# Performance work log

Measured on AMD Instinct MI355X. Metric: run time of the kernel, lower is better.

The kernel has to match this reference:

```python
import jax, jax.numpy as jnp
import numpy as np

G = 2            # num_codevector_groups
C = 320          # num_codevectors_per_group
VQ_DIM = 256     # codevector_dim
HID = 512        # conv_dimensions[-1]
TAU = 2.0


def setup_inputs() -> dict:
    key = jax.random.key(0)
    k1, k2, k3, k4 = jax.random.split(key, 4)
    B, S = 16, 2048
    x = jax.random.normal(k1, (B, S, HID), dtype=jnp.float32)
    # iid Gumbel(0,1) noise, same shape as flattened logits [B*S*G, C]
    u = jax.random.uniform(k2, (B * S * G, C), dtype=jnp.float32, minval=1e-6, maxval=1.0 - 1e-6)
    gumbel = -jnp.log(-jnp.log(u))
    Wq = jax.random.normal(k3, (G * C, HID), dtype=jnp.float32) * (1.0 / np.sqrt(HID))
    bq = jnp.zeros((G * C,), dtype=jnp.float32)
    codevectors = jax.random.uniform(k4, (1, G * C, VQ_DIM // G), dtype=jnp.float32)
    return {"x": x, "gumbel": gumbel, "Wq": Wq, "bq": bq, "codevectors": codevectors}


def reference(x, gumbel, Wq, bq, codevectors):
    B, S, H = x.shape
    N = B * S
    logits = jnp.einsum('bsh,gh->bsg', x, Wq) + bq          # [B, S, G*C]
    logits = logits.reshape(N * G, C)

    # hard gumbel-softmax (training path) with straight-through estimator
    y_soft = jax.nn.softmax((logits + gumbel) / TAU, axis=-1)
    idx = jnp.argmax(y_soft, axis=-1)
    y_hard = jax.nn.one_hot(idx, C, dtype=y_soft.dtype)
    probs = y_hard + y_soft - jax.lax.stop_gradient(y_soft)  # [N*G, C]

    # perplexity from plain softmax of logits (no gumbel noise), masked_token_idx=None
    soft_probs = jax.nn.softmax(logits.reshape(N, G, C), axis=-1)
    mean_p = soft_probs.mean(axis=0)                          # [G, C]
    perplexity = jnp.exp(-jnp.sum(mean_p * jnp.log(mean_p + 1e-7), axis=-1)).sum()

    # weighted sum over codes per group == einsum (same math as broadcast*sum in torch)
    cv = codevectors.reshape(G, C, VQ_DIM // G)               # [G, C, d]
    sel = jnp.einsum('ngc,gcd->ngd', probs.reshape(N, G, C), cv)
    selected_codes = sel.reshape(B, S, VQ_DIM)
    return selected_codes, perplexity
```

## Files before the change

kernel.cpp:

```cpp
#include <hip/hip_runtime.h>
#include <hip/hip_fp16.h>

#define HID 512
#define GC  640
#define CC  320
#define GG  2
#define DHALF 128
#define MARGIN 0.004f
#define FB 4

typedef __attribute__((ext_vector_type(8))) _Float16 half8;
typedef __attribute__((ext_vector_type(4))) float float4v;

__device__ __forceinline__ void gload16(const void* g, void* l) {
    __builtin_amdgcn_global_load_lds(
        (const __attribute__((address_space(1))) void*)(unsigned long long)g,
        (__attribute__((address_space(3))) void*)(unsigned)(unsigned long long)l,
        16, 0, 0);
}

__global__ __launch_bounds__(256) void zero_misc(float* meanAcc, int* cnt) {
    for (int i = threadIdx.x; i < GC; i += 256) meanAcc[i] = 0.f;
    if (threadIdx.x < 2) cnt[threadIdx.x] = 0;
}

__global__ __launch_bounds__(256) void convert_f16(
    const float* __restrict__ in, unsigned short* __restrict__ out, int n8)
{
    int i = blockIdx.x * 256 + threadIdx.x;
    if (i >= n8) return;
    const float4* p = (const float4*)in + (size_t)i * 2;
    float4 v0 = p[0], v1 = p[1];
    float f[8] = {v0.x, v0.y, v0.z, v0.w, v1.x, v1.y, v1.z, v1.w};
    unsigned r[4];
#pragma unroll
    for (int j = 0; j < 4; ++j) {
        __half2 hh = __float22half2_rn(make_float2(f[2*j], f[2*j+1]));
        r[j] = __builtin_bit_cast(unsigned, hh);
    }
    uint4 o = {r[0], r[1], r[2], r[3]};
    *(uint4*)(out + (size_t)i * 8) = o;
}

__global__ __launch_bounds__(512, 4) void fused(
    const float* __restrict__ X, const unsigned short* __restrict__ Wh,
    const float* __restrict__ bq, const float* __restrict__ gum,
    const float* __restrict__ cv, float* __restrict__ out,
    float* __restrict__ meanAcc, int* __restrict__ cnt,
    int* __restrict__ flags0, int* __restrict__ flags1)
{
    __shared__ __align__(16) unsigned short As[2][4096];
    __shared__ __align__(16) unsigned short Bs[2][10240];
    __shared__ float bqs[CC];
    __shared__ float smean[CC];

    const int tid  = threadIdx.x;
    const int lane = tid & 63;
    const int wid  = tid >> 6;
    const int lq   = lane & 15;
    const int q    = lane >> 4;

    int bid = blockIdx.x;
    int nwg = gridDim.x;
    int swz = ((nwg & 7) == 0) ? (bid & 7) * (nwg >> 3) + (bid >> 3) : bid;
    const int g    = swz & 1;
    const int tok0 = (swz >> 1) * 128;
    int* flagsg = g ? flags1 : flags0;

    for (int i = tid; i < CC; i += 512) { bqs[i] = bq[g * CC + i]; smean[i] = 0.f; }

    const int iss0 = wid, iss1 = wid + 8, iss2 = wid + 16;
    const int c0 = (iss0 * 64 + lane) ^ (((iss0 * 64 + lane) >> 3) & 7);
    const int c1 = (iss1 * 64 + lane) ^ (((iss1 * 64 + lane) >> 3) & 7);
    const int c2 = (iss2 * 64 + lane) ^ (((iss2 * 64 + lane) >> 3) & 7);
    const unsigned short* srcB0 = Wh + ((size_t)(g * CC + (c0 >> 2))) * HID + (c0 & 3) * 8;
    const unsigned short* srcB1 = Wh + ((size_t)(g * CC + (c1 >> 2))) * HID + (c1 & 3) * 8;
    const unsigned short* srcB2 = Wh + ((size_t)(g * CC + (c2 >> 2))) * HID + (c2 & 3) * 8;

    const int ca = tid ^ ((tid >> 3) & 7);
    const float* xsrc = X + (size_t)(tok0 + (ca >> 2)) * HID + (ca & 3) * 8;

    int aoff = ((wid * 16 + lq) << 6) + (q << 4);
    aoff ^= ((aoff >> 7) & 7) << 4;
    int boff = (lq << 6) + (q << 4);
    boff ^= (((lq >> 1) & 7) << 4);

    float4v acc[20];
#pragma unroll
    for (int j = 0; j < 20; ++j) acc[j] = (float4v){0.f, 0.f, 0.f, 0.f};

    {
        float4 xa = *(const float4*)xsrc;
        float4 xb = *(const float4*)(xsrc + 4);
        gload16(srcB0, &Bs[0][iss0 * 512]);
        gload16(srcB1, &Bs[0][iss1 * 512]);
        if (wid < 4) gload16(srcB2, &Bs[0][iss2 * 512]);
        half8 h;
        h[0] = (_Float16)xa.x; h[1] = (_Float16)xa.y;
        h[2] = (_Float16)xa.z; h[3] = (_Float16)xa.w;
        h[4] = (_Float16)xb.x; h[5] = (_Float16)xb.y;
        h[6] = (_Float16)xb.z; h[7] = (_Float16)xb.w;
        *(half8*)&As[0][tid * 8] = h;
    }
    __syncthreads();

    int cur = 0;
    for (int kk = 0; kk < 16; ++kk) {
        const int k0n = ((kk + 1) & 15) * 32;
        float4 nxa = *(const float4*)(xsrc + k0n);
        float4 nxb = *(const float4*)(xsrc + k0n + 4);
        gload16(srcB0 + k0n, &Bs[cur ^ 1][iss0 * 512]);
        gload16(srcB1 + k0n, &Bs[cur ^ 1][iss1 * 512]);
        if (wid < 4) gload16(srcB2 + k0n, &Bs[cur ^ 1][iss2 * 512]);

        half8 a = *(const half8*)((const char*)&As[cur][0] + aoff);
        const char* bbase = (const char*)&Bs[cur][0] + boff;
#pragma unroll
        for (int j = 0; j < 20; ++j) {
            half8 b = *(const half8*)(bbase + j * 1024);
            acc[j] = __builtin_amdgcn_mfma_f32_16x16x32_f16(a, b, acc[j], 0, 0, 0);
        }

        half8 h;
        h[0] = (_Float16)nxa.x; h[1] = (_Float16)nxa.y;
        h[2] = (_Float16)nxa.z; h[3] = (_Float16)nxa.w;
        h[4] = (_Float16)nxb.x; h[5] = (_Float16)nxb.y;
        h[6] = (_Float16)nxb.z; h[7] = (_Float16)nxb.w;
        *(half8*)&As[cur ^ 1][tid * 8] = h;

        __syncthreads();
        cur ^= 1;
    }

    float macc[20];
#pragma unroll
    for (int j = 0; j < 20; ++j) macc[j] = 0.f;

#pragma unroll
    for (int r = 0; r < 4; ++r) {
        const int rowL  = wid * 16 + q * 4 + r;
        const int tglob = tok0 + rowL;
        const float* grow = gum + ((size_t)tglob * GG + g) * CC;
        float s = 0.f;
        float b = -3.0e38f; int bi = 0; float s2 = -3.0e38f;
#pragma unroll
        for (int j = 0; j < 20; ++j) {
            const int c = j * 16 + lq;
            float lg = acc[j][r] + bqs[c];
            float v  = lg + grow[c];
            if (v > b)       { s2 = b; b = v; bi = c; }
            else if (v > s2) { s2 = v; }
            s += __expf(lg);
        }
#pragma unroll
        for (int m = 1; m < 16; m <<= 1) {
            float os  = __shfl_xor(s,  m, 64);
            float ob  = __shfl_xor(b,  m, 64);
            int   obi = __shfl_xor(bi, m, 64);
            float os2 = __shfl_xor(s2, m, 64);
            s += os;
            if (ob > b || (ob == b && obi < bi)) { s2 = fmaxf(os2, b); b = ob; bi = obi; }
            else                                 { s2 = fmaxf(s2, ob); }
        }
        float inv = 1.f / s;
#pragma unroll
        for (int j = 0; j < 20; ++j)
            macc[j] += __expf(acc[j][r] + bqs[j * 16 + lq]) * inv;

        if (lq == 0 && (b - s2) < MARGIN) {
            int p = atomicAdd(&cnt[g], 1);
            flagsg[p] = tglob;
        }
        const float* cvp = cv + ((size_t)(g * CC + bi)) * DHALF + lq * 8;
        float4 c0v = *(const float4*)cvp;
        float4 c1v = *(const float4*)(cvp + 4);
        float* op = out + (size_t)tglob * 256 + g * DHALF + lq * 8;
        *(float4*)op       = c0v;
        *(float4*)(op + 4) = c1v;
    }
#pragma unroll
    for (int j = 0; j < 20; ++j) {
        macc[j] += __shfl_xor(macc[j], 16, 64);
        macc[j] += __shfl_xor(macc[j], 32, 64);
    }
    if (lane < 16) {
#pragma unroll
        for (int j = 0; j < 20; ++j)
            atomicAdd(&smean[j * 16 + lq], macc[j]);
    }
    __syncthreads();
    for (int i = tid; i < CC; i += 512)
        atomicAdd(&meanAcc[g * CC + i], smean[i]);
}

__global__ __launch_bounds__(320) void fixup(
    const float* __restrict__ X, const float* __restrict__ W,
    const float* __restrict__ bq, const float* __restrict__ gum,
    const float* __restrict__ cv, float* __restrict__ out,
    const int* __restrict__ flags0, const int* __restrict__ flags1,
    const int* __restrict__ cnt)
{
    __shared__ float xs[FB][HID];
    __shared__ float vals[FB][CC];
    __shared__ int stok[FB];
    const int tid = threadIdx.x;
    const int n0 = cnt[0], n1 = cnt[1];
    const int nb0 = (n0 + FB - 1) / FB;
    const int nb1 = (n1 + FB - 1) / FB;

    for (int bb = blockIdx.x; bb < nb0 + nb1; bb += gridDim.x) {
        const int g    = (bb < nb0) ? 0 : 1;
        const int lb   = (bb < nb0) ? bb : bb - nb0;
        const int n    = g ? n1 : n0;
        const int* fl  = g ? flags1 : flags0;
        const int r0   = lb * FB;
        const int nr   = (n - r0 < FB) ? (n - r0) : FB;

        if (tid < FB) {
            int idx = r0 + tid;
            if (idx >= n) idx = n - 1;
            stok[tid] = fl[idx];
        }
        __syncthreads();
        for (int i = tid; i < FB * (HID / 4); i += 320) {
            int r = i >> 7, k4 = i & 127;
            *(float4*)&xs[r][k4 * 4] = *(const float4*)(X + (size_t)stok[r] * HID + k4 * 4);
        }
        __syncthreads();

        {
            const int c = tid;
            if (c < CC) {
                const float* wr = W + (size_t)(g * CC + c) * HID;
                float acc[FB];
#pragma unroll
                for (int r = 0; r < FB; ++r) acc[r] = 0.f;
                for (int k4 = 0; k4 < HID / 4; ++k4) {
                    float4 w4 = *(const float4*)(wr + k4 * 4);
#pragma unroll
                    for (int r = 0; r < FB; ++r) {
                        float4 xv = *(const float4*)&xs[r][k4 * 4];
                        acc[r] = fmaf(xv.x, w4.x, acc[r]);
                        acc[r] = fmaf(xv.y, w4.y, acc[r]);
                        acc[r] = fmaf(xv.z, w4.z, acc[r]);
                        acc[r] = fmaf(xv.w, w4.w, acc[r]);
                    }
                }
                float bias = bq[g * CC + c];
#pragma unroll
                for (int r = 0; r < FB; ++r)
                    vals[r][c] = acc[r] + bias + gum[((size_t)stok[r] * GG + g) * CC + c];
            }
        }
        __syncthreads();

        const int lane = tid & 63;
        const int wv   = tid >> 6;
        if (wv < FB) {
            const int r = wv;
            if (r < nr) {
                float b = -3.0e38f; int bi = 0;
#pragma unroll
                for (int j = 0; j < 5; ++j) {
                    int c = lane + j * 64;
                    float v = vals[r][c];
                    if (v > b || (v == b && c < bi)) { b = v; bi = c; }
                }
#pragma unroll
                for (int m = 32; m; m >>= 1) {
                    float ob = __shfl_xor(b, m, 64);
                    int  obi = __shfl_xor(bi, m, 64);
                    if (ob > b || (ob == b && obi < bi)) { b = ob; bi = obi; }
                }
                int tok = stok[r];
                float2 cvv = *(const float2*)(cv + ((size_t)(g * CC + bi)) * DHALF + lane * 2);
                *(float2*)(out + (size_t)tok * 256 + g * DHALF + lane * 2) = cvv;
            }
        }
        __syncthreads();
    }
}

__global__ __launch_bounds__(256) void perpk(
    const float* __restrict__ meanAcc, float* __restrict__ outp, int ntot)
{
    __shared__ float red0[256];
    __shared__ float red1[256];
    const float invn = 1.f / (float)ntot;
    float h0 = 0.f, h1 = 0.f;
    for (int c = threadIdx.x; c < CC; c += 256) {
        float p0 = meanAcc[c]      * invn;
        float p1 = meanAcc[CC + c] * invn;
        h0 -= p0 * logf(p0 + 1e-7f);
        h1 -= p1 * logf(p1 + 1e-7f);
    }
    red0[threadIdx.x] = h0; red1[threadIdx.x] = h1;
    __syncthreads();
    for (int s = 128; s; s >>= 1) {
        if (threadIdx.x < (unsigned)s) {
            red0[threadIdx.x] += red0[threadIdx.x + s];
            red1[threadIdx.x] += red1[threadIdx.x + s];
        }
        __syncthreads();
    }
    if (threadIdx.x == 0) outp[0] = expf(red0[0]) + expf(red1[0]);
}

extern "C" void kernel_launch(void* const* d_in, const int* in_sizes, int n_in,
                              void* d_out, int out_size, void* d_ws, size_t ws_size,
                              hipStream_t stream) {
    const float* x      = (const float*)d_in[0];
    const float* gumbel = (const float*)d_in[1];
    const float* Wq     = (const float*)d_in[2];
    const float* bq     = (const float*)d_in[3];
    const float* cv     = (const float*)d_in[4];
    float* out = (float*)d_out;

    const int NT = in_sizes[0] / HID;

    char* wsc = (char*)d_ws;
    float* meanAcc = (float*)wsc;
    int*   cnt     = (int*)(wsc + 2560);
    int*   flags0  = (int*)(wsc + 4096);
    int*   flags1  = (int*)(wsc + 135168);
    unsigned short* Wh = (unsigned short*)(wsc + 266240);

    zero_misc<<<1, 256, 0, stream>>>(meanAcc, cnt);
    convert_f16<<<(GC * HID / 8 + 255) / 256, 256, 0, stream>>>(Wq, Wh, GC * HID / 8);

    const int nwg = (NT / 128) * 2;
    fused<<<nwg, 512, 0, stream>>>(x, Wh, bq, gumbel, cv, out,
                                   meanAcc, cnt, flags0, flags1);

    fixup<<<256, 320, 0, stream>>>(x, Wq, bq, gumbel, cv, out, flags0, flags1, cnt);
    perpk<<<1, 256, 0, stream>>>(meanAcc, out + (size_t)out_size - 1, NT);
}
```

Measured before the change: 123.8 us.

## Transpose logits through LDS so gumbel reads are contiguous per thread

The epilogue now writes the MFMA accumulator tile into a shared-memory staging buffer that aliases the GEMM double buffers. Each thread then processes 20 contiguous codes of one row, so gumbel noise is read with float4 vector loads instead of strided scalar loads. The exponentials are kept in registers and reused for the mean-probability accumulation, and the cross-lane shuffle reduction of macc is replaced with direct shared atomics. This adds a barrier per row pass and LDS traffic in exchange for coalesced gumbel loads and less recomputation of exp.

```diff
diff --git a/kernel.cpp b/kernel.cpp
--- a/kernel.cpp
+++ b/kernel.cpp
@@ -8,6 +8,7 @@
 #define DHALF 128
 #define MARGIN 0.004f
 #define FB 4
+#define REPLD 324
 
 typedef __attribute__((ext_vector_type(8))) _Float16 half8;
 typedef __attribute__((ext_vector_type(4))) float float4v;
@@ -49,8 +50,10 @@
     float* __restrict__ meanAcc, int* __restrict__ cnt,
     int* __restrict__ flags0, int* __restrict__ flags1)
 {
-    __shared__ __align__(16) unsigned short As[2][4096];
-    __shared__ __align__(16) unsigned short Bs[2][10240];
+    __shared__ __align__(16) char lds[57344];
+    unsigned short* As0 = (unsigned short*)lds;
+    unsigned short* Bs0 = (unsigned short*)(lds + 16384);
+    float* rep = (float*)lds;
     __shared__ float bqs[CC];
     __shared__ float smean[CC];
 
@@ -70,12 +73,12 @@
     for (int i = tid; i < CC; i += 512) { bqs[i] = bq[g * CC + i]; smean[i] = 0.f; }
 
     const int iss0 = wid, iss1 = wid + 8, iss2 = wid + 16;
-    const int c0 = (iss0 * 64 + lane) ^ (((iss0 * 64 + lane) >> 3) & 7);
-    const int c1 = (iss1 * 64 + lane) ^ (((iss1 * 64 + lane) >> 3) & 7);
-    const int c2 = (iss2 * 64 + lane) ^ (((iss2 * 64 + lane) >> 3) & 7);
-    const unsigned short* srcB0 = Wh + ((size_t)(g * CC + (c0 >> 2))) * HID + (c0 & 3) * 8;
-    const unsigned short* srcB1 = Wh + ((size_t)(g * CC + (c1 >> 2))) * HID + (c1 & 3) * 8;
-    const unsigned short* srcB2 = Wh + ((size_t)(g * CC + (c2 >> 2))) * HID + (c2 & 3) * 8;
+    const int c0i = (iss0 * 64 + lane) ^ (((iss0 * 64 + lane) >> 3) & 7);
+    const int c1i = (iss1 * 64 + lane) ^ (((iss1 * 64 + lane) >> 3) & 7);
+    const int c2i = (iss2 * 64 + lane) ^ (((iss2 * 64 + lane) >> 3) & 7);
+    const unsigned short* srcB0 = Wh + ((size_t)(g * CC + (c0i >> 2))) * HID + (c0i & 3) * 8;
+    const unsigned short* srcB1 = Wh + ((size_t)(g * CC + (c1i >> 2))) * HID + (c1i & 3) * 8;
+    const unsigned short* srcB2 = Wh + ((size_t)(g * CC + (c2i >> 2))) * HID + (c2i & 3) * 8;
 
     const int ca = tid ^ ((tid >> 3) & 7);
     const float* xsrc = X + (size_t)(tok0 + (ca >> 2)) * HID + (ca & 3) * 8;
@@ -92,15 +95,15 @@
     {
         float4 xa = *(const float4*)xsrc;
         float4 xb = *(const float4*)(xsrc + 4);
-        gload16(srcB0, &Bs[0][iss0 * 512]);
-        gload16(srcB1, &Bs[0][iss1 * 512]);
-        if (wid < 4) gload16(srcB2, &Bs[0][iss2 * 512]);
+        gload16(srcB0, Bs0 + iss0 * 512);
+        gload16(srcB1, Bs0 + iss1 * 512);
+        if (wid < 4) gload16(srcB2, Bs0 + iss2 * 512);
         half8 h;
         h[0] = (_Float16)xa.x; h[1] = (_Float16)xa.y;
         h[2] = (_Float16)xa.z; h[3] = (_Float16)xa.w;
         h[4] = (_Float16)xb.x; h[5] = (_Float16)xb.y;
         h[6] = (_Float16)xb.z; h[7] = (_Float16)xb.w;
-        *(half8*)&As[0][tid * 8] = h;
+        *(half8*)&As0[tid * 8] = h;
     }
     __syncthreads();
 
@@ -109,12 +112,13 @@
         const int k0n = ((kk + 1) & 15) * 32;
         float4 nxa = *(const float4*)(xsrc + k0n);
         float4 nxb = *(const float4*)(xsrc + k0n + 4);
-        gload16(srcB0 + k0n, &Bs[cur ^ 1][iss0 * 512]);
-        gload16(srcB1 + k0n, &Bs[cur ^ 1][iss1 * 512]);
-        if (wid < 4) gload16(srcB2 + k0n, &Bs[cur ^ 1][iss2 * 512]);
-
-        half8 a = *(const half8*)((const char*)&As[cur][0] + aoff);
-        const char* bbase = (const char*)&Bs[cur][0] + boff;
+        unsigned short* Bnext = Bs0 + (cur ^ 1) * 10240;
+        gload16(srcB0 + k0n, Bnext + iss0 * 512);
+        gload16(srcB1 + k0n, Bnext + iss1 * 512);
+        if (wid < 4) gload16(srcB2 + k0n, Bnext + iss2 * 512);
+
+        half8 a = *(const half8*)((const char*)(As0 + cur * 4096) + aoff);
+        const char* bbase = (const char*)(Bs0 + cur * 10240) + boff;
 #pragma unroll
         for (int j = 0; j < 20; ++j) {
             half8 b = *(const half8*)(bbase + j * 1024);
@@ -126,7 +130,7 @@
         h[2] = (_Float16)nxa.z; h[3] = (_Float16)nxa.w;
         h[4] = (_Float16)nxb.x; h[5] = (_Float16)nxb.y;
         h[6] = (_Float16)nxb.z; h[7] = (_Float16)nxb.w;
-        *(half8*)&As[cur ^ 1][tid * 8] = h;
+        *(half8*)&As0[(cur ^ 1) * 4096 + tid * 8] = h;
 
         __syncthreads();
         cur ^= 1;
@@ -135,22 +139,39 @@
     float macc[20];
 #pragma unroll
     for (int j = 0; j < 20; ++j) macc[j] = 0.f;
-
-#pragma unroll
+    const int gg = tid >> 4;
+    const int lql = tid & 15;
+    const int cb = lql * 20;
+
     for (int r = 0; r < 4; ++r) {
-        const int rowL  = wid * 16 + q * 4 + r;
+        const int slot = wid * 4 + q;
+#pragma unroll
+        for (int j = 0; j < 20; ++j)
+            rep[slot * REPLD + j * 16 + lq] = acc[j][r] + bqs[j * 16 + lq];
+        __syncthreads();
+
+        const int rowL  = (gg >> 2) * 16 + (gg & 3) * 4 + r;
         const int tglob = tok0 + rowL;
-        const float* grow = gum + ((size_t)tglob * GG + g) * CC;
+        const float* grow = gum + ((size_t)tglob * GG + g) * CC + cb;
+        const float* rrow = rep + gg * REPLD + cb;
+
+        float le[20];
         float s = 0.f;
         float b = -3.0e38f; int bi = 0; float s2 = -3.0e38f;
 #pragma unroll
-        for (int j = 0; j < 20; ++j) {
-            const int c = j * 16 + lq;
-            float lg = acc[j][r] + bqs[c];
-            float v  = lg + grow[c];
-            if (v > b)       { s2 = b; b = v; bi = c; }
-            else if (v > s2) { s2 = v; }
-            s += __expf(lg);
+        for (int jj = 0; jj < 5; ++jj) {
+            float4 lv = *(const float4*)(rrow + jj * 4);
+            float4 gv = *(const float4*)(grow + jj * 4);
+            float lf[4] = {lv.x, lv.y, lv.z, lv.w};
+            float gf[4] = {gv.x, gv.y, gv.z, gv.w};
+#pragma unroll
+            for (int t = 0; t < 4; ++t) {
+                int j = jj * 4 + t;
+                float v = lf[t] + gf[t];
+                if (v > b)       { s2 = b; b = v; bi = cb + j; }
+                else if (v > s2) { s2 = v; }
+                le[j] = __expf(lf[t]); s += le[j];
+            }
         }
 #pragma unroll
         for (int m = 1; m < 16; m <<= 1) {
@@ -164,30 +185,24 @@
         }
         float inv = 1.f / s;
 #pragma unroll
-        for (int j = 0; j < 20; ++j)
-            macc[j] += __expf(acc[j][r] + bqs[j * 16 + lq]) * inv;
-
-        if (lq == 0 && (b - s2) < MARGIN) {
+        for (int j = 0; j < 20; ++j) macc[j] += le[j] * inv;
+
+        if (lql == 0 && (b - s2) < MARGIN) {
             int p = atomicAdd(&cnt[g], 1);
             flagsg[p] = tglob;
         }
-        const float* cvp = cv + ((size_t)(g * CC + bi)) * DHALF + lq * 8;
+        const float* cvp = cv + ((size_t)(g * CC + bi)) * DHALF + lql * 8;
         float4 c0v = *(const float4*)cvp;
         float4 c1v = *(const float4*)(cvp + 4);
-        float* op = out + (size_t)tglob * 256 + g * DHALF + lq * 8;
+        float* op = out + (size_t)tglob * 256 + g * DHALF + lql * 8;
         *(float4*)op       = c0v;
         *(float4*)(op + 4) = c1v;
-    }
-#pragma unroll
-    for (int j = 0; j < 20; ++j) {
-        macc[j] += __shfl_xor(macc[j], 16, 64);
-        macc[j] += __shfl_xor(macc[j], 32, 64);
-    }
-    if (lane < 16) {
-#pragma unroll
-        for (int j = 0; j < 20; ++j)
-            atomicAdd(&smean[j * 16 + lq], macc[j]);
-    }
+        __syncthreads();
+    }
+
+#pragma unroll
+    for (int j = 0; j < 20; ++j)
+        atomicAdd(&smean[cb + j], macc[j]);
     __syncthreads();
     for (int i = tid; i < CC; i += 512)
         atomicAdd(&meanAcc[g * CC + i], smean[i]);
```

Result: slower. 180.4 us (+45.8%).
